# Kernel tuning notes

Hardware: AMD Instinct MI355X
Metric: run time of the kernel (lower is better)

The kernel has to match this reference:

```python
import jax, jax.numpy as jnp
import numpy as np

N_NODES = 50000
N_EDGES = 800000
IN_DIM = 128
ADD = 8
HIDDEN = 256
OUT_DIM = 128


def gcn_conv(x, src, dst, W, b, n_nodes):
    """PyG GCNConv: linear -> sym-normalized scatter-add with self-loops -> bias."""
    loop = jnp.arange(n_nodes, dtype=src.dtype)
    s = jnp.concatenate([src, loop])
    d = jnp.concatenate([dst, loop])
    deg = jax.ops.segment_sum(jnp.ones(s.shape[0], dtype=x.dtype), d, num_segments=n_nodes)
    dinv = jnp.where(deg > 0, jax.lax.rsqrt(deg), 0.0)
    norm = dinv[s] * dinv[d]                       # [E+N]
    h = x @ W                                      # [N, F_out]
    msg = h[s] * norm[:, None]                     # [E+N, F_out]
    out = jax.ops.segment_sum(msg, d, num_segments=n_nodes)
    return out + b


def prelu(x, a):
    return jnp.where(x >= 0, x, a * x)


def setup_inputs() -> dict:
    key = jax.random.key(0)
    ks = jax.random.split(key, 8)
    x = jax.random.normal(ks[0], (N_NODES, IN_DIM), dtype=jnp.float32)
    edge_index = jax.random.randint(ks[1], (2, N_EDGES), 0, N_NODES, dtype=jnp.int64)
    id_vec = jax.random.normal(ks[2], (ADD,), dtype=jnp.float32)
    # Glorot-ish init for linear weights, PReLU slope 0.25 (torch default)
    W1 = jax.random.normal(ks[3], (IN_DIM + ADD, HIDDEN), dtype=jnp.float32) * 0.05
    b1 = jnp.zeros((HIDDEN,), dtype=jnp.float32)
    a1 = jnp.full((HIDDEN,), 0.25, dtype=jnp.float32)
    W2 = jax.random.normal(ks[4], (HIDDEN, OUT_DIM), dtype=jnp.float32) * 0.05
    b2 = jnp.zeros((OUT_DIM,), dtype=jnp.float32)
    a2 = jnp.full((OUT_DIM,), 0.25, dtype=jnp.float32)
    return {"x": x, "edge_index": edge_index, "id": id_vec,
            "W1": W1, "b1": b1, "a1": a1, "W2": W2, "b2": b2, "a2": a2}


def reference(x, edge_index, id, W1, b1, a1, W2, b2, a2):
    n = x.shape[0]
    src, dst = edge_index[0], edge_index[1]
    # tile id vector onto every node and concat along features
    xi = jnp.concatenate([x, jnp.broadcast_to(id[None, :], (n, id.shape[0]))], axis=1)
    h = gcn_conv(xi, src, dst, W1, b1, n)
    h = prelu(h, a1)
    h = gcn_conv(h, src, dst, W2, b2, n)
    h = prelu(h, a2)
    return h
```

## Files before the change

kernel.cpp:

```cpp
#include <hip/hip_runtime.h>


constexpr int NN = 50000;
constexpr int NE = 800000;
constexpr int NBUCK = 196;
constexpr int TILE = 2048;
constexpr int NSCAT = (NE + TILE - 1) / TILE;

typedef __attribute__((ext_vector_type(8))) short short8;
typedef __attribute__((ext_vector_type(4))) float floatx4;

__device__ inline void bsplit(float v, unsigned short& hi, unsigned short& lo) {
  unsigned u = __float_as_uint(v);
  hi = (unsigned short)(u >> 16);
  float rem = v - __uint_as_float(u & 0xffff0000u);
  lo = (unsigned short)(__float_as_uint(rem) >> 16);
}

__device__ inline unsigned short bf16_rtne(float v) {
  unsigned u = __float_as_uint(v);
  return (unsigned short)((u + 0x7fffu + ((u >> 16) & 1u)) >> 16);
}

__device__ inline float bflo(unsigned u) { return __uint_as_float(u << 16); }
__device__ inline float bfhi(unsigned u) { return __uint_as_float(u & 0xffff0000u); }


__global__ __launch_bounds__(256) void tile_count_kernel(const int* __restrict__ ei,
                                                         int* __restrict__ tilecnt) {
  __shared__ int h[NBUCK];
  int t = threadIdx.x;
  for (int i = t; i < NBUCK; i += 256) h[i] = 0;
  __syncthreads();
  int base = blockIdx.x * TILE;
  int end = base + TILE; if (end > NE) end = NE;
  for (int e = base + t; e < end; e += 256) atomicAdd(&h[ei[NE + e] >> 8], 1);
  __syncthreads();
  for (int i = t; i < NBUCK; i += 256) tilecnt[blockIdx.x * NBUCK + i] = h[i];
}

__global__ __launch_bounds__(256) void tile_scan_a_kernel(const int* __restrict__ tilecnt,
                                                          int* __restrict__ tpre,
                                                          int* __restrict__ bcnt) {
  __shared__ int sm[256];
  int b = blockIdx.x, t = threadIdx.x;
  int i0 = 2 * t, i1 = 2 * t + 1;
  int v0 = (i0 < NSCAT) ? tilecnt[i0 * NBUCK + b] : 0;
  int v1 = (i1 < NSCAT) ? tilecnt[i1 * NBUCK + b] : 0;
  int s = v0 + v1;
  sm[t] = s;
  __syncthreads();
  for (int off = 1; off < 256; off <<= 1) {
    int u = (t >= off) ? sm[t - off] : 0;
    __syncthreads();
    sm[t] += u;
    __syncthreads();
  }
  int ex = sm[t] - s;
  if (i0 < NSCAT) tpre[i0 * NBUCK + b] = ex;
  if (i1 < NSCAT) tpre[i1 * NBUCK + b] = ex + v0;
  if (t == 255) bcnt[b] = sm[255];
}

__global__ void bucket_base_kernel(const int* __restrict__ bcnt, int* __restrict__ bbase) {
  __shared__ int sm[256];
  int t = threadIdx.x;
  int v = (t < NBUCK) ? bcnt[t] : 0;
  sm[t] = v;
  __syncthreads();
  for (int off = 1; off < 256; off <<= 1) {
    int u = (t >= off) ? sm[t - off] : 0;
    __syncthreads();
    sm[t] += u;
    __syncthreads();
  }
  if (t < NBUCK) bbase[t] = sm[t] - v;
}

__global__ __launch_bounds__(256) void bucket_scatter_kernel(
    const int* __restrict__ ei, const int* __restrict__ tilecnt,
    const int* __restrict__ tpre, const int* __restrict__ bbase,
    unsigned* __restrict__ ebuf) {
  __shared__ int lbase[NBUCK], gb[NBUCK], lcur[NBUCK], ssc[256];
  __shared__ unsigned stage[TILE];
  int t = threadIdx.x;
  int tile = blockIdx.x;
  int base = tile * TILE;
  int cntTile = NE - base; if (cntTile > TILE) cntTile = TILE;
  int h = (t < NBUCK) ? tilecnt[tile * NBUCK + t] : 0;
  ssc[t] = h;
  __syncthreads();
  for (int off = 1; off < 256; off <<= 1) {
    int u = (t >= off) ? ssc[t - off] : 0;
    __syncthreads();
    ssc[t] += u;
    __syncthreads();
  }
  if (t < NBUCK) {
    int ex = ssc[t] - h;
    lbase[t] = ex;
    lcur[t] = ex;
    gb[t] = bbase[t] + tpre[tile * NBUCK + t];
  }
  __syncthreads();
  for (int e = base + t; e < base + cntTile; e += 256) {
    int s = ei[e];
    int d = ei[NE + e];
    int b = d >> 8;
    int pos = atomicAdd(&lcur[b], 1);
    stage[pos] = ((unsigned)(d & 255) << 16) | (unsigned)s;
  }
  __syncthreads();
  for (int i = t; i < cntTile; i += 256) {
    int lo = 0, hi = NBUCK - 1;
    while (lo < hi) {
      int mid = (lo + hi + 1) >> 1;
      if (lbase[mid] <= i) lo = mid; else hi = mid - 1;
    }
    ebuf[gb[lo] + (i - lbase[lo])] = stage[i];
  }
}

__global__ __launch_bounds__(256) void bucket_csr_kernel(
    const unsigned* __restrict__ ebuf, const int* __restrict__ bbase,
    const int* __restrict__ bcnt, int* __restrict__ offs, int* __restrict__ col,
    float* __restrict__ dinv) {
  __shared__ int cnt[256], cur[256], sums[256];
  int b = blockIdx.x, t = threadIdx.x;
  int node0 = b << 8;
  cnt[t] = 0;
  __syncthreads();
  int g0 = bbase[b], g1 = g0 + bcnt[b];
  for (int i = g0 + t; i < g1; i += 256) atomicAdd(&cnt[ebuf[i] >> 16], 1);
  __syncthreads();
  int c = cnt[t];
  sums[t] = c;
  __syncthreads();
  for (int off = 1; off < 256; off <<= 1) {
    int u = (t >= off) ? sums[t - off] : 0;
    __syncthreads();
    sums[t] += u;
    __syncthreads();
  }
  int ex = sums[t] - c;
  cur[t] = ex;
  int node = node0 + t;
  if (node < NN) {
    offs[node] = g0 + ex;
    dinv[node] = rsqrtf((float)(c + 1));
  }
  __syncthreads();
  for (int i = g0 + t; i < g1; i += 256) {
    unsigned v = ebuf[i];
    int pos = atomicAdd(&cur[v >> 16], 1);
    col[g0 + pos] = (int)(v & 0xffffu);
  }
  if (b == 0 && t == 0) offs[NN] = NE;
}

__global__ __launch_bounds__(256) void post_csr_kernel(
    const float* __restrict__ x, const float* __restrict__ dinv,
    const int* __restrict__ offs, const int* __restrict__ col,
    unsigned short* __restrict__ xsb, float* __restrict__ Svec) {
  int id = blockIdx.x * 256 + threadIdx.x;
  if (id < NN * 32) {
    float dd = dinv[id >> 5];
    float4 v = ((const float4*)x)[id];
    ushort4 o;
    o.x = bf16_rtne(v.x * dd);
    o.y = bf16_rtne(v.y * dd);
    o.z = bf16_rtne(v.z * dd);
    o.w = bf16_rtne(v.w * dd);
    ((ushort4*)xsb)[id] = o;
  } else {
    int d = id - NN * 32;
    if (d < NN) {
      float s = 0.f;
      int end = offs[d + 1];
      for (int p = offs[d]; p < end; ++p) s += dinv[col[p]];
      float dd = dinv[d];
      Svec[d] = dd * (dd + s);
    }
  }
}

template <int K, int N>
__device__ inline void pack_one(const float* __restrict__ W, unsigned short* __restrict__ Bhi,
                                unsigned short* __restrict__ Blo, int id) {
  constexpr int KC = K / 32;
  int j = id & 7;
  int lane = (id >> 3) & 63;
  int rest = id >> 9;
  int c = rest % KC;
  int nt = rest / KC;
  int k = c * 32 + (lane >> 4) * 8 + j;
  int n = nt * 16 + (lane & 15);
  unsigned short hi, lo;
  bsplit(W[(size_t)k * N + n], hi, lo);
  Bhi[id] = hi;
  Blo[id] = lo;
}

__global__ void prep_weights_kernel(const float* __restrict__ W1, const float* __restrict__ W2,
                                    const float* __restrict__ idv,
                                    unsigned short* __restrict__ B1hi, unsigned short* __restrict__ B1lo,
                                    unsigned short* __restrict__ B2hi, unsigned short* __restrict__ B2lo,
                                    float* __restrict__ cvec) {
  int id = blockIdx.x * 256 + threadIdx.x;
  if (id < 32768) {
    pack_one<128, 256>(W1, B1hi, B1lo, id);
  } else if (id < 65536) {
    pack_one<256, 128>(W2, B2hi, B2lo, id - 32768);
  } else if (id < 65536 + 256) {
    int m = id - 65536;
    float c = 0.f;
#pragma unroll
    for (int j = 0; j < 8; ++j) c += idv[j] * W1[(128 + j) * 256 + m];
    cvec[m] = c;
  }
}

template <int MODE>
__global__ __launch_bounds__(256) void agg_kernel(
    const unsigned short* __restrict__ in, const float* __restrict__ dinv,
    const int* __restrict__ offs, const int* __restrict__ col,
    const float* __restrict__ bias, const float* __restrict__ alpha,
    unsigned short* __restrict__ outhi, unsigned short* __restrict__ outlo,
    float* __restrict__ outf) {
  const uint2* inb = (const uint2*)in;
  int t = threadIdx.x;
  int node = blockIdx.x * 4 + (t >> 6);
  int lane = t & 63;
  int r = lane & 31;
  int half = lane >> 5;
  int beg = offs[node], end = offs[node + 1];

  float4 a0 = make_float4(0.f, 0.f, 0.f, 0.f);
  float4 a1 = make_float4(0.f, 0.f, 0.f, 0.f);
  float4 a2 = make_float4(0.f, 0.f, 0.f, 0.f);
  float4 a3 = make_float4(0.f, 0.f, 0.f, 0.f);
  int p = beg + half;
  for (; p + 14 < end; p += 16) {
    int s0 = col[p];      int s1 = col[p + 2];
    int s2 = col[p + 4];  int s3 = col[p + 6];
    int s4 = col[p + 8];  int s5 = col[p + 10];
    int s6 = col[p + 12]; int s7 = col[p + 14];
    uint2 v0 = inb[(size_t)s0 * 32 + r];
    uint2 v1 = inb[(size_t)s1 * 32 + r];
    uint2 v2 = inb[(size_t)s2 * 32 + r];
    uint2 v3 = inb[(size_t)s3 * 32 + r];
    uint2 v4 = inb[(size_t)s4 * 32 + r];
    uint2 v5 = inb[(size_t)s5 * 32 + r];
    uint2 v6 = inb[(size_t)s6 * 32 + r];
    uint2 v7 = inb[(size_t)s7 * 32 + r];
    a0.x += bflo(v0.x); a0.y += bfhi(v0.x); a0.z += bflo(v0.y); a0.w += bfhi(v0.y);
    a1.x += bflo(v1.x); a1.y += bfhi(v1.x); a1.z += bflo(v1.y); a1.w += bfhi(v1.y);
    a2.x += bflo(v2.x); a2.y += bfhi(v2.x); a2.z += bflo(v2.y); a2.w += bfhi(v2.y);
    a3.x += bflo(v3.x); a3.y += bfhi(v3.x); a3.z += bflo(v3.y); a3.w += bfhi(v3.y);
    a0.x += bflo(v4.x); a0.y += bfhi(v4.x); a0.z += bflo(v4.y); a0.w += bfhi(v4.y);
    a1.x += bflo(v5.x); a1.y += bfhi(v5.x); a1.z += bflo(v5.y); a1.w += bfhi(v5.y);
    a2.x += bflo(v6.x); a2.y += bfhi(v6.x); a2.z += bflo(v6.y); a2.w += bfhi(v6.y);
    a3.x += bflo(v7.x); a3.y += bfhi(v7.x); a3.z += bflo(v7.y); a3.w += bfhi(v7.y);
  }
  for (; p + 2 < end; p += 4) {
    int s0 = col[p];
    int s1 = col[p + 2];
    uint2 v0 = inb[(size_t)s0 * 32 + r];
    uint2 v1 = inb[(size_t)s1 * 32 + r];
    a0.x += bflo(v0.x); a0.y += bfhi(v0.x); a0.z += bflo(v0.y); a0.w += bfhi(v0.y);
    a1.x += bflo(v1.x); a1.y += bfhi(v1.x); a1.z += bflo(v1.y); a1.w += bfhi(v1.y);
  }
  if (p < end) {
    uint2 v0 = inb[(size_t)col[p] * 32 + r];
    a0.x += bflo(v0.x); a0.y += bfhi(v0.x); a0.z += bflo(v0.y); a0.w += bfhi(v0.y);
  }
  float4 acc = make_float4((a0.x + a1.x) + (a2.x + a3.x), (a0.y + a1.y) + (a2.y + a3.y),
                           (a0.z + a1.z) + (a2.z + a3.z), (a0.w + a1.w) + (a2.w + a3.w));
  acc.x += __shfl_xor(acc.x, 32);
  acc.y += __shfl_xor(acc.y, 32);
  acc.z += __shfl_xor(acc.z, 32);
  acc.w += __shfl_xor(acc.w, 32);

  float dd = dinv[node];
  if (half == 0) {
    uint2 sv = inb[(size_t)node * 32 + r];
    acc.x = dd * (acc.x + bflo(sv.x));
    acc.y = dd * (acc.y + bfhi(sv.x));
    acc.z = dd * (acc.z + bflo(sv.y));
    acc.w = dd * (acc.w + bfhi(sv.y));
    if (MODE == 0) {
      ushort4 h4, l4;
      bsplit(acc.x, h4.x, l4.x);
      bsplit(acc.y, h4.y, l4.y);
      bsplit(acc.z, h4.z, l4.z);
      bsplit(acc.w, h4.w, l4.w);
      ((ushort4*)outhi)[(size_t)node * 32 + r] = h4;
      ((ushort4*)outlo)[(size_t)node * 32 + r] = l4;
    } else {
      float4 b = ((const float4*)bias)[r];
      float4 al = ((const float4*)alpha)[r];
      acc.x += b.x; acc.y += b.y; acc.z += b.z; acc.w += b.w;
      acc.x = (acc.x >= 0.f) ? acc.x : al.x * acc.x;
      acc.y = (acc.y >= 0.f) ? acc.y : al.y * acc.y;
      acc.z = (acc.z >= 0.f) ? acc.z : al.z * acc.z;
      acc.w = (acc.w >= 0.f) ? acc.w : al.w * acc.w;
      ((float4*)outf)[(size_t)node * 32 + r] = acc;
    }
  }
}

__global__ __launch_bounds__(256) void gemm_fused_kernel(
    const unsigned short* __restrict__ Ahi, const unsigned short* __restrict__ Alo,
    const unsigned short* __restrict__ B1hi, const unsigned short* __restrict__ B1lo,
    const unsigned short* __restrict__ B2hi, const unsigned short* __restrict__ B2lo,
    const float* __restrict__ Svec, const float* __restrict__ cvec,
    const float* __restrict__ bias, const float* __restrict__ alpha,
    const float* __restrict__ dinv, unsigned short* __restrict__ h2b) {
  constexpr int K1 = 128, KC1 = 4, NT1 = 16;
  constexpr int KC2 = 8, NT2 = 8;
  __shared__ __attribute__((aligned(16))) char smem[4 * 16384];

  int wave = threadIdx.x >> 6;
  int lane = threadIdx.x & 63;
  int row0 = blockIdx.x * 64 + wave * 16;
  if (row0 >= NN) return;
  int m = lane & 15, quad = lane >> 4;
  char* wb = smem + wave * 16384;

  short8 ah[KC1], al[KC1];
  const unsigned short* ap = Ahi + (size_t)(row0 + m) * K1 + quad * 8;
  const unsigned short* alp = Alo + (size_t)(row0 + m) * K1 + quad * 8;
#pragma unroll
  for (int c = 0; c < KC1; ++c) {
    ah[c] = *(const short8*)(ap + c * 32);
    al[c] = *(const short8*)(alp + c * 32);
  }
  float sv[4];
#pragma unroll
  for (int i = 0; i < 4; ++i) sv[i] = Svec[row0 + quad * 4 + i];

#pragma unroll 1
  for (int nt = 0; nt < NT1; ++nt) {
    floatx4 acc = {0.f, 0.f, 0.f, 0.f};
#pragma unroll
    for (int c = 0; c < KC1; ++c) {
      short8 bh = *(const short8*)(B1hi + ((size_t)(nt * KC1 + c) * 64 + lane) * 8);
      short8 bl = *(const short8*)(B1lo + ((size_t)(nt * KC1 + c) * 64 + lane) * 8);
      acc = __builtin_amdgcn_mfma_f32_16x16x32_bf16(ah[c], bh, acc, 0, 0, 0);
      acc = __builtin_amdgcn_mfma_f32_16x16x32_bf16(ah[c], bl, acc, 0, 0, 0);
      acc = __builtin_amdgcn_mfma_f32_16x16x32_bf16(al[c], bh, acc, 0, 0, 0);
    }
    int c0 = nt * 16 + m;
    float cv = cvec[c0], bb = bias[c0], aa = alpha[c0];
#pragma unroll
    for (int i = 0; i < 4; ++i) {
      float v = acc[i] + sv[i] * cv + bb;
      v = (v >= 0.f) ? v : aa * v;
      unsigned short hi, lo;
      bsplit(v, hi, lo);
      int row16 = quad * 4 + i;
      int off = row16 * 512 + ((c0 * 2) ^ ((row16 & 7) << 4));
      *(unsigned short*)(wb + off) = hi;
      *(unsigned short*)(wb + 8192 + off) = lo;
    }
  }

  short8 ah2[KC2], al2[KC2];
#pragma unroll
  for (int c = 0; c < KC2; ++c) {
    int off = m * 512 + ((c * 64 + quad * 16) ^ ((m & 7) << 4));
    ah2[c] = *(const short8*)(wb + off);
    al2[c] = *(const short8*)(wb + 8192 + off);
  }
  float dv[4];
#pragma unroll
  for (int i = 0; i < 4; ++i) dv[i] = dinv[row0 + quad * 4 + i];

#pragma unroll 1
  for (int nt = 0; nt < NT2; ++nt) {
    floatx4 acc = {0.f, 0.f, 0.f, 0.f};
#pragma unroll
    for (int c = 0; c < KC2; ++c) {
      short8 bh = *(const short8*)(B2hi + ((size_t)(nt * KC2 + c) * 64 + lane) * 8);
      short8 bl = *(const short8*)(B2lo + ((size_t)(nt * KC2 + c) * 64 + lane) * 8);
      acc = __builtin_amdgcn_mfma_f32_16x16x32_bf16(ah2[c], bh, acc, 0, 0, 0);
      acc = __builtin_amdgcn_mfma_f32_16x16x32_bf16(ah2[c], bl, acc, 0, 0, 0);
      acc = __builtin_amdgcn_mfma_f32_16x16x32_bf16(al2[c], bh, acc, 0, 0, 0);
    }
    int c0 = nt * 16 + m;
#pragma unroll
    for (int i = 0; i < 4; ++i) {
      int r = row0 + quad * 4 + i;
      h2b[(size_t)r * 128 + c0] = bf16_rtne(acc[i] * dv[i]);
    }
  }
}

extern "C" void kernel_launch(void* const* d_in, const int* in_sizes, int n_in,
                              void* d_out, int out_size, void* d_ws, size_t ws_size,
                              hipStream_t stream) {
  const float* x = (const float*)d_in[0];
  const int* ei = (const int*)d_in[1];
  const float* idv = (const float*)d_in[2];
  const float* W1 = (const float*)d_in[3];
  const float* b1 = (const float*)d_in[4];
  const float* a1 = (const float*)d_in[5];
  const float* W2 = (const float*)d_in[6];
  const float* b2 = (const float*)d_in[7];
  const float* a2 = (const float*)d_in[8];
  float* out = (float*)d_out;

  char* w = (char*)d_ws;
  size_t off = 0;
  auto alloc = [&](size_t bytes) -> void* {
    void* p = w + off;
    off += bytes;
    off = (off + 255) & ~(size_t)255;
    return p;
  };
  int* tilecnt = (int*)alloc((size_t)NSCAT * NBUCK * 4);
  int* tpre = (int*)alloc((size_t)NSCAT * NBUCK * 4);
  int* bbase = (int*)alloc((size_t)NBUCK * 4);
  int* bcnt = (int*)alloc((size_t)NBUCK * 4);
  unsigned* ebuf = (unsigned*)alloc((size_t)NE * 4);
  float* dinv = (float*)alloc((size_t)NN * 4);
  float* Svec = (float*)alloc((size_t)NN * 4);
  int* offs = (int*)alloc((size_t)(NN + 1) * 4);
  int* col = (int*)alloc((size_t)NE * 4);
  float* cvec = (float*)alloc(256 * 4);
  unsigned short* xsb = (unsigned short*)alloc((size_t)NN * 128 * 2);
  unsigned short* aggxhi = (unsigned short*)alloc((size_t)NN * 128 * 2);
  unsigned short* aggxlo = (unsigned short*)alloc((size_t)NN * 128 * 2);
  unsigned short* h2b = (unsigned short*)alloc((size_t)NN * 128 * 2);
  unsigned short* B1hi = (unsigned short*)alloc(128 * 256 * 2);
  unsigned short* B1lo = (unsigned short*)alloc(128 * 256 * 2);
  unsigned short* B2hi = (unsigned short*)alloc(256 * 128 * 2);
  unsigned short* B2lo = (unsigned short*)alloc(256 * 128 * 2);

  tile_count_kernel<<<NSCAT, 256, 0, stream>>>(ei, tilecnt);
  tile_scan_a_kernel<<<NBUCK, 256, 0, stream>>>(tilecnt, tpre, bcnt);
  bucket_base_kernel<<<1, 256, 0, stream>>>(bcnt, bbase);
  bucket_scatter_kernel<<<NSCAT, 256, 0, stream>>>(ei, tilecnt, tpre, bbase, ebuf);
  bucket_csr_kernel<<<NBUCK, 256, 0, stream>>>(ebuf, bbase, bcnt, offs, col, dinv);

  prep_weights_kernel<<<(65536 + 256 + 255) / 256, 256, 0, stream>>>(
      W1, W2, idv, B1hi, B1lo, B2hi, B2lo, cvec);
  post_csr_kernel<<<(NN * 32 + NN + 255) / 256, 256, 0, stream>>>(
      x, dinv, offs, col, xsb, Svec);

  agg_kernel<0><<<NN / 4, 256, 0, stream>>>(xsb, dinv, offs, col, nullptr, nullptr,
                                            aggxhi, aggxlo, nullptr);

  gemm_fused_kernel<<<(NN + 63) / 64, 256, 0, stream>>>(
      aggxhi, aggxlo, B1hi, B1lo, B2hi, B2lo, Svec, cvec, b1, a1, dinv, h2b);

  agg_kernel<1><<<NN / 4, 256, 0, stream>>>(h2b, dinv, offs, col, b2, a2,
                                            nullptr, nullptr, out);
}
```

Baseline: 256.4 us.

## Chain fused GEMMs in registers via transposed MFMA, removing LDS staging

Swaps the MFMA operand roles so the first GEMM produces a transposed output tile whose per-lane layout matches the B-operand layout of the second GEMM. W1 is repacked with a permuted column order so that each pair of 16-column tiles feeds one 32-wide K chunk of the second GEMM directly from registers. This drops the per-wave 16KB LDS staging buffer and lets output stores be vectorized ushort4 writes. In exchange it keeps eight accumulator tiles live across the loop, which raises register pressure, and it adds a launch_bounds occupancy hint.

```diff
diff --git a/kernel.cpp b/kernel.cpp
--- a/kernel.cpp
+++ b/kernel.cpp
@@ -201,6 +201,22 @@
   Blo[id] = lo;
 }
 
+__device__ inline void pack_w1(const float* __restrict__ W, unsigned short* __restrict__ Bhi,
+                               unsigned short* __restrict__ Blo, int id) {
+  int j = id & 7;
+  int lane = (id >> 3) & 63;
+  int rest = id >> 9;
+  int c = rest & 3;
+  int nt = rest >> 2;
+  int k = c * 32 + (lane >> 4) * 8 + j;
+  int r = lane & 15;
+  int n = 32 * (nt >> 1) + 8 * (r >> 2) + 4 * (nt & 1) + (r & 3);
+  unsigned short hi, lo;
+  bsplit(W[(size_t)k * 256 + n], hi, lo);
+  Bhi[id] = hi;
+  Blo[id] = lo;
+}
+
 __global__ void prep_weights_kernel(const float* __restrict__ W1, const float* __restrict__ W2,
                                     const float* __restrict__ idv,
                                     unsigned short* __restrict__ B1hi, unsigned short* __restrict__ B1lo,
@@ -208,7 +224,7 @@
                                     float* __restrict__ cvec) {
   int id = blockIdx.x * 256 + threadIdx.x;
   if (id < 32768) {
-    pack_one<128, 256>(W1, B1hi, B1lo, id);
+    pack_w1(W1, B1hi, B1lo, id);
   } else if (id < 65536) {
     pack_one<256, 128>(W2, B2hi, B2lo, id - 32768);
   } else if (id < 65536 + 256) {
@@ -309,90 +325,89 @@
   }
 }
 
-__global__ __launch_bounds__(256) void gemm_fused_kernel(
+__global__ __launch_bounds__(256, 4) void gemm_fused_kernel(
     const unsigned short* __restrict__ Ahi, const unsigned short* __restrict__ Alo,
     const unsigned short* __restrict__ B1hi, const unsigned short* __restrict__ B1lo,
     const unsigned short* __restrict__ B2hi, const unsigned short* __restrict__ B2lo,
     const float* __restrict__ Svec, const float* __restrict__ cvec,
     const float* __restrict__ bias, const float* __restrict__ alpha,
     const float* __restrict__ dinv, unsigned short* __restrict__ h2b) {
-  constexpr int K1 = 128, KC1 = 4, NT1 = 16;
-  constexpr int KC2 = 8, NT2 = 8;
-  __shared__ __attribute__((aligned(16))) char smem[4 * 16384];
-
+  constexpr int K1 = 128, KC1 = 4;
   int wave = threadIdx.x >> 6;
   int lane = threadIdx.x & 63;
   int row0 = blockIdx.x * 64 + wave * 16;
   if (row0 >= NN) return;
   int m = lane & 15, quad = lane >> 4;
-  char* wb = smem + wave * 16384;
-
-  short8 ah[KC1], al[KC1];
-  const unsigned short* ap = Ahi + (size_t)(row0 + m) * K1 + quad * 8;
-  const unsigned short* alp = Alo + (size_t)(row0 + m) * K1 + quad * 8;
+  int node = row0 + m;
+
+  short8 gh[KC1], gl[KC1];
+  const unsigned short* gp = Ahi + (size_t)node * K1 + quad * 8;
+  const unsigned short* glp = Alo + (size_t)node * K1 + quad * 8;
 #pragma unroll
   for (int c = 0; c < KC1; ++c) {
-    ah[c] = *(const short8*)(ap + c * 32);
-    al[c] = *(const short8*)(alp + c * 32);
-  }
-  float sv[4];
-#pragma unroll
-  for (int i = 0; i < 4; ++i) sv[i] = Svec[row0 + quad * 4 + i];
+    gh[c] = *(const short8*)(gp + c * 32);
+    gl[c] = *(const short8*)(glp + c * 32);
+  }
+  float sv = Svec[node];
+  float dv = dinv[node];
+
+  floatx4 acc2[8];
+#pragma unroll
+  for (int n = 0; n < 8; ++n) acc2[n] = {0.f, 0.f, 0.f, 0.f};
 
 #pragma unroll 1
-  for (int nt = 0; nt < NT1; ++nt) {
-    floatx4 acc = {0.f, 0.f, 0.f, 0.f};
-#pragma unroll
-    for (int c = 0; c < KC1; ++c) {
-      short8 bh = *(const short8*)(B1hi + ((size_t)(nt * KC1 + c) * 64 + lane) * 8);
-      short8 bl = *(const short8*)(B1lo + ((size_t)(nt * KC1 + c) * 64 + lane) * 8);
-      acc = __builtin_amdgcn_mfma_f32_16x16x32_bf16(ah[c], bh, acc, 0, 0, 0);
-      acc = __builtin_amdgcn_mfma_f32_16x16x32_bf16(ah[c], bl, acc, 0, 0, 0);
-      acc = __builtin_amdgcn_mfma_f32_16x16x32_bf16(al[c], bh, acc, 0, 0, 0);
-    }
-    int c0 = nt * 16 + m;
-    float cv = cvec[c0], bb = bias[c0], aa = alpha[c0];
+  for (int t = 0; t < 8; ++t) {
+    float p0[4], p1[4];
+#pragma unroll
+    for (int P = 0; P < 2; ++P) {
+      int nt = 2 * t + P;
+      floatx4 acc = {0.f, 0.f, 0.f, 0.f};
+#pragma unroll
+      for (int c = 0; c < KC1; ++c) {
+        short8 wh = *(const short8*)(B1hi + ((size_t)(nt * KC1 + c) * 64 + lane) * 8);
+        short8 wl = *(const short8*)(B1lo + ((size_t)(nt * KC1 + c) * 64 + lane) * 8);
+        acc = __builtin_amdgcn_mfma_f32_16x16x32_bf16(wh, gh[c], acc, 0, 0, 0);
+        acc = __builtin_amdgcn_mfma_f32_16x16x32_bf16(wl, gh[c], acc, 0, 0, 0);
+        acc = __builtin_amdgcn_mfma_f32_16x16x32_bf16(wh, gl[c], acc, 0, 0, 0);
+      }
+      int cb = t * 32 + quad * 8 + P * 4;
+      floatx4 cvv = *(const floatx4*)(cvec + cb);
+      floatx4 bbv = *(const floatx4*)(bias + cb);
+      floatx4 aav = *(const floatx4*)(alpha + cb);
+#pragma unroll
+      for (int i = 0; i < 4; ++i) {
+        float v = acc[i] + sv * cvv[i] + bbv[i];
+        v = (v >= 0.f) ? v : aav[i] * v;
+        if (P == 0) p0[i] = v; else p1[i] = v;
+      }
+    }
+    short8 bh2, bl2;
 #pragma unroll
     for (int i = 0; i < 4; ++i) {
-      float v = acc[i] + sv[i] * cv + bb;
-      v = (v >= 0.f) ? v : aa * v;
       unsigned short hi, lo;
-      bsplit(v, hi, lo);
-      int row16 = quad * 4 + i;
-      int off = row16 * 512 + ((c0 * 2) ^ ((row16 & 7) << 4));
-      *(unsigned short*)(wb + off) = hi;
-      *(unsigned short*)(wb + 8192 + off) = lo;
-    }
-  }
-
-  short8 ah2[KC2], al2[KC2];
-#pragma unroll
-  for (int c = 0; c < KC2; ++c) {
-    int off = m * 512 + ((c * 64 + quad * 16) ^ ((m & 7) << 4));
-    ah2[c] = *(const short8*)(wb + off);
-    al2[c] = *(const short8*)(wb + 8192 + off);
-  }
-  float dv[4];
-#pragma unroll
-  for (int i = 0; i < 4; ++i) dv[i] = dinv[row0 + quad * 4 + i];
-
-#pragma unroll 1
-  for (int nt = 0; nt < NT2; ++nt) {
-    floatx4 acc = {0.f, 0.f, 0.f, 0.f};
-#pragma unroll
-    for (int c = 0; c < KC2; ++c) {
-      short8 bh = *(const short8*)(B2hi + ((size_t)(nt * KC2 + c) * 64 + lane) * 8);
-      short8 bl = *(const short8*)(B2lo + ((size_t)(nt * KC2 + c) * 64 + lane) * 8);
-      acc = __builtin_amdgcn_mfma_f32_16x16x32_bf16(ah2[c], bh, acc, 0, 0, 0);
-      acc = __builtin_amdgcn_mfma_f32_16x16x32_bf16(ah2[c], bl, acc, 0, 0, 0);
-      acc = __builtin_amdgcn_mfma_f32_16x16x32_bf16(al2[c], bh, acc, 0, 0, 0);
-    }
-    int c0 = nt * 16 + m;
-#pragma unroll
-    for (int i = 0; i < 4; ++i) {
-      int r = row0 + quad * 4 + i;
-      h2b[(size_t)r * 128 + c0] = bf16_rtne(acc[i] * dv[i]);
-    }
+      bsplit(p0[i], hi, lo);
+      bh2[i] = (short)hi; bl2[i] = (short)lo;
+      bsplit(p1[i], hi, lo);
+      bh2[4 + i] = (short)hi; bl2[4 + i] = (short)lo;
+    }
+#pragma unroll
+    for (int n = 0; n < 8; ++n) {
+      short8 a2h = *(const short8*)(B2hi + ((size_t)(n * 8 + t) * 64 + lane) * 8);
+      short8 a2l = *(const short8*)(B2lo + ((size_t)(n * 8 + t) * 64 + lane) * 8);
+      acc2[n] = __builtin_amdgcn_mfma_f32_16x16x32_bf16(a2h, bh2, acc2[n], 0, 0, 0);
+      acc2[n] = __builtin_amdgcn_mfma_f32_16x16x32_bf16(a2l, bh2, acc2[n], 0, 0, 0);
+      acc2[n] = __builtin_amdgcn_mfma_f32_16x16x32_bf16(a2h, bl2, acc2[n], 0, 0, 0);
+    }
+  }
+
+#pragma unroll
+  for (int n = 0; n < 8; ++n) {
+    ushort4 o;
+    o.x = bf16_rtne(acc2[n][0] * dv);
+    o.y = bf16_rtne(acc2[n][1] * dv);
+    o.z = bf16_rtne(acc2[n][2] * dv);
+    o.w = bf16_rtne(acc2[n][3] * dv);
+    *(ushort4*)(h2b + (size_t)node * 128 + n * 16 + quad * 4) = o;
   }
 }
 
```

New measurement: 274.4 us. 7.0% more time.

## Fuse first-layer neighbor aggregation into the fused GEMM kernel via LDS staging

Applied to the files above, without the earlier changes.

The separate first aggregation kernel, which wrote hi/lo bf16 split buffers to global memory, is removed. Each wave of the GEMM kernel now gathers its own 16 rows from the CSR, splits the results into hi/lo and stores them in a swizzled LDS tile, then loads the MFMA A operands from LDS. This drops one launch and the global write plus read-back of two 50000x128 bf16 buffers. In exchange, each wave walks 16 nodes one after another, so the gather has less parallelism per wave and its latency is harder to hide, and it now runs inside a kernel with high register pressure.

```diff
diff --git a/kernel.cpp b/kernel.cpp
--- a/kernel.cpp
+++ b/kernel.cpp
@@ -220,12 +220,10 @@
   }
 }
 
-template <int MODE>
 __global__ __launch_bounds__(256) void agg_kernel(
     const unsigned short* __restrict__ in, const float* __restrict__ dinv,
     const int* __restrict__ offs, const int* __restrict__ col,
     const float* __restrict__ bias, const float* __restrict__ alpha,
-    unsigned short* __restrict__ outhi, unsigned short* __restrict__ outlo,
     float* __restrict__ outf) {
   const uint2* inb = (const uint2*)in;
   int t = threadIdx.x;
@@ -283,57 +281,117 @@
 
   float dd = dinv[node];
   if (half == 0) {
-    uint2 sv = inb[(size_t)node * 32 + r];
-    acc.x = dd * (acc.x + bflo(sv.x));
-    acc.y = dd * (acc.y + bfhi(sv.x));
-    acc.z = dd * (acc.z + bflo(sv.y));
-    acc.w = dd * (acc.w + bfhi(sv.y));
-    if (MODE == 0) {
+    uint2 slf = inb[(size_t)node * 32 + r];
+    acc.x = dd * (acc.x + bflo(slf.x));
+    acc.y = dd * (acc.y + bfhi(slf.x));
+    acc.z = dd * (acc.z + bflo(slf.y));
+    acc.w = dd * (acc.w + bfhi(slf.y));
+    float4 b = ((const float4*)bias)[r];
+    float4 al = ((const float4*)alpha)[r];
+    acc.x += b.x; acc.y += b.y; acc.z += b.z; acc.w += b.w;
+    acc.x = (acc.x >= 0.f) ? acc.x : al.x * acc.x;
+    acc.y = (acc.y >= 0.f) ? acc.y : al.y * acc.y;
+    acc.z = (acc.z >= 0.f) ? acc.z : al.z * acc.z;
+    acc.w = (acc.w >= 0.f) ? acc.w : al.w * acc.w;
+    ((float4*)outf)[(size_t)node * 32 + r] = acc;
+  }
+}
+
+__global__ __launch_bounds__(256) void gemm_fused_kernel(
+    const unsigned short* __restrict__ xsb, const int* __restrict__ offs,
+    const int* __restrict__ col,
+    const unsigned short* __restrict__ B1hi, const unsigned short* __restrict__ B1lo,
+    const unsigned short* __restrict__ B2hi, const unsigned short* __restrict__ B2lo,
+    const float* __restrict__ Svec, const float* __restrict__ cvec,
+    const float* __restrict__ bias, const float* __restrict__ alpha,
+    const float* __restrict__ dinv, unsigned short* __restrict__ h2b) {
+  constexpr int KC1 = 4, NT1 = 16;
+  constexpr int KC2 = 8, NT2 = 8;
+  __shared__ __attribute__((aligned(16))) char smem[4 * 16384];
+
+  int wave = threadIdx.x >> 6;
+  int lane = threadIdx.x & 63;
+  int row0 = blockIdx.x * 64 + wave * 16;
+  if (row0 >= NN) return;
+  int m = lane & 15, quad = lane >> 4;
+  int r = lane & 31, half = lane >> 5;
+  char* wb = smem + wave * 16384;
+  const uint2* inb = (const uint2*)xsb;
+
+#pragma unroll 1
+  for (int i = 0; i < 16; ++i) {
+    int node = row0 + i;
+    int beg = offs[node], end = offs[node + 1];
+    float4 a0 = make_float4(0.f, 0.f, 0.f, 0.f);
+    float4 a1 = make_float4(0.f, 0.f, 0.f, 0.f);
+    float4 a2 = make_float4(0.f, 0.f, 0.f, 0.f);
+    float4 a3 = make_float4(0.f, 0.f, 0.f, 0.f);
+    int p = beg + half;
+    for (; p + 14 < end; p += 16) {
+      int s0 = col[p];      int s1 = col[p + 2];
+      int s2 = col[p + 4];  int s3 = col[p + 6];
+      int s4 = col[p + 8];  int s5 = col[p + 10];
+      int s6 = col[p + 12]; int s7 = col[p + 14];
+      uint2 v0 = inb[(size_t)s0 * 32 + r];
+      uint2 v1 = inb[(size_t)s1 * 32 + r];
+      uint2 v2 = inb[(size_t)s2 * 32 + r];
+      uint2 v3 = inb[(size_t)s3 * 32 + r];
+      uint2 v4 = inb[(size_t)s4 * 32 + r];
+      uint2 v5 = inb[(size_t)s5 * 32 + r];
+      uint2 v6 = inb[(size_t)s6 * 32 + r];
+      uint2 v7 = inb[(size_t)s7 * 32 + r];
+      a0.x += bflo(v0.x); a0.y += bfhi(v0.x); a0.z += bflo(v0.y); a0.w += bfhi(v0.y);
+      a1.x += bflo(v1.x); a1.y += bfhi(v1.x); a1.z += bflo(v1.y); a1.w += bfhi(v1.y);
+      a2.x += bflo(v2.x); a2.y += bfhi(v2.x); a2.z += bflo(v2.y); a2.w += bfhi(v2.y);
+      a3.x += bflo(v3.x); a3.y += bfhi(v3.x); a3.z += bflo(v3.y); a3.w += bfhi(v3.y);
+      a0.x += bflo(v4.x); a0.y += bfhi(v4.x); a0.z += bflo(v4.y); a0.w += bfhi(v4.y);
+      a1.x += bflo(v5.x); a1.y += bfhi(v5.x); a1.z += bflo(v5.y); a1.w += bfhi(v5.y);
+      a2.x += bflo(v6.x); a2.y += bfhi(v6.x); a2.z += bflo(v6.y); a2.w += bfhi(v6.y);
+      a3.x += bflo(v7.x); a3.y += bfhi(v7.x); a3.z += bflo(v7.y); a3.w += bfhi(v7.y);
+    }
+    for (; p + 2 < end; p += 4) {
+      int s0 = col[p];
+      int s1 = col[p + 2];
+      uint2 v0 = inb[(size_t)s0 * 32 + r];
+      uint2 v1 = inb[(size_t)s1 * 32 + r];
+      a0.x += bflo(v0.x); a0.y += bfhi(v0.x); a0.z += bflo(v0.y); a0.w += bfhi(v0.y);
+      a1.x += bflo(v1.x); a1.y += bfhi(v1.x); a1.z += bflo(v1.y); a1.w += bfhi(v1.y);
+    }
+    if (p < end) {
+      uint2 v0 = inb[(size_t)col[p] * 32 + r];
+      a0.x += bflo(v0.x); a0.y += bfhi(v0.x); a0.z += bflo(v0.y); a0.w += bfhi(v0.y);
+    }
+    float4 acc = make_float4((a0.x + a1.x) + (a2.x + a3.x), (a0.y + a1.y) + (a2.y + a3.y),
+                             (a0.z + a1.z) + (a2.z + a3.z), (a0.w + a1.w) + (a2.w + a3.w));
+    acc.x += __shfl_xor(acc.x, 32);
+    acc.y += __shfl_xor(acc.y, 32);
+    acc.z += __shfl_xor(acc.z, 32);
+    acc.w += __shfl_xor(acc.w, 32);
+
+    float dd = dinv[node];
+    if (half == 0) {
+      uint2 slf = inb[(size_t)node * 32 + r];
+      acc.x = dd * (acc.x + bflo(slf.x));
+      acc.y = dd * (acc.y + bfhi(slf.x));
+      acc.z = dd * (acc.z + bflo(slf.y));
+      acc.w = dd * (acc.w + bfhi(slf.y));
       ushort4 h4, l4;
       bsplit(acc.x, h4.x, l4.x);
       bsplit(acc.y, h4.y, l4.y);
       bsplit(acc.z, h4.z, l4.z);
       bsplit(acc.w, h4.w, l4.w);
-      ((ushort4*)outhi)[(size_t)node * 32 + r] = h4;
-      ((ushort4*)outlo)[(size_t)node * 32 + r] = l4;
-    } else {
-      float4 b = ((const float4*)bias)[r];
-      float4 al = ((const float4*)alpha)[r];
-      acc.x += b.x; acc.y += b.y; acc.z += b.z; acc.w += b.w;
-      acc.x = (acc.x >= 0.f) ? acc.x : al.x * acc.x;
-      acc.y = (acc.y >= 0.f) ? acc.y : al.y * acc.y;
-      acc.z = (acc.z >= 0.f) ? acc.z : al.z * acc.z;
-      acc.w = (acc.w >= 0.f) ? acc.w : al.w * acc.w;
-      ((float4*)outf)[(size_t)node * 32 + r] = acc;
-    }
-  }
-}
-
-__global__ __launch_bounds__(256) void gemm_fused_kernel(
-    const unsigned short* __restrict__ Ahi, const unsigned short* __restrict__ Alo,
-    const unsigned short* __restrict__ B1hi, const unsigned short* __restrict__ B1lo,
-    const unsigned short* __restrict__ B2hi, const unsigned short* __restrict__ B2lo,
-    const float* __restrict__ Svec, const float* __restrict__ cvec,
-    const float* __restrict__ bias, const float* __restrict__ alpha,
-    const float* __restrict__ dinv, unsigned short* __restrict__ h2b) {
-  constexpr int K1 = 128, KC1 = 4, NT1 = 16;
-  constexpr int KC2 = 8, NT2 = 8;
-  __shared__ __attribute__((aligned(16))) char smem[4 * 16384];
-
-  int wave = threadIdx.x >> 6;
-  int lane = threadIdx.x & 63;
-  int row0 = blockIdx.x * 64 + wave * 16;
-  if (row0 >= NN) return;
-  int m = lane & 15, quad = lane >> 4;
-  char* wb = smem + wave * 16384;
+      int loff = i * 256 + ((r * 8) ^ ((i & 7) << 4));
+      *(ushort4*)(wb + loff) = h4;
+      *(ushort4*)(wb + 4096 + loff) = l4;
+    }
+  }
 
   short8 ah[KC1], al[KC1];
-  const unsigned short* ap = Ahi + (size_t)(row0 + m) * K1 + quad * 8;
-  const unsigned short* alp = Alo + (size_t)(row0 + m) * K1 + quad * 8;
 #pragma unroll
   for (int c = 0; c < KC1; ++c) {
-    ah[c] = *(const short8*)(ap + c * 32);
-    al[c] = *(const short8*)(alp + c * 32);
+    int loff = m * 256 + ((c * 64 + quad * 16) ^ ((m & 7) << 4));
+    ah[c] = *(const short8*)(wb + loff);
+    al[c] = *(const short8*)(wb + 4096 + loff);
   }
   float sv[4];
 #pragma unroll
@@ -390,8 +448,8 @@
     int c0 = nt * 16 + m;
 #pragma unroll
     for (int i = 0; i < 4; ++i) {
-      int r = row0 + quad * 4 + i;
-      h2b[(size_t)r * 128 + c0] = bf16_rtne(acc[i] * dv[i]);
+      int rr = row0 + quad * 4 + i;
+      h2b[(size_t)rr * 128 + c0] = bf16_rtne(acc[i] * dv[i]);
     }
   }
 }
@@ -429,8 +487,6 @@
   int* col = (int*)alloc((size_t)NE * 4);
   float* cvec = (float*)alloc(256 * 4);
   unsigned short* xsb = (unsigned short*)alloc((size_t)NN * 128 * 2);
-  unsigned short* aggxhi = (unsigned short*)alloc((size_t)NN * 128 * 2);
-  unsigned short* aggxlo = (unsigned short*)alloc((size_t)NN * 128 * 2);
   unsigned short* h2b = (unsigned short*)alloc((size_t)NN * 128 * 2);
   unsigned short* B1hi = (unsigned short*)alloc(128 * 256 * 2);
   unsigned short* B1lo = (unsigned short*)alloc(128 * 256 * 2);
@@ -448,12 +504,8 @@
   post_csr_kernel<<<(NN * 32 + NN + 255) / 256, 256, 0, stream>>>(
       x, dinv, offs, col, xsb, Svec);
 
-  agg_kernel<0><<<NN / 4, 256, 0, stream>>>(xsb, dinv, offs, col, nullptr, nullptr,
-                                            aggxhi, aggxlo, nullptr);
-
   gemm_fused_kernel<<<(NN + 63) / 64, 256, 0, stream>>>(
-      aggxhi, aggxlo, B1hi, B1lo, B2hi, B2lo, Svec, cvec, b1, a1, dinv, h2b);
-
-  agg_kernel<1><<<NN / 4, 256, 0, stream>>>(h2b, dinv, offs, col, b2, a2,
-                                            nullptr, nullptr, out);
-}
+      xsb, offs, col, B1hi, B1lo, B2hi, B2lo, Svec, cvec, b1, a1, dinv, h2b);
+
+  agg_kernel<<<NN / 4, 256, 0, stream>>>(h2b, dinv, offs, col, b2, a2, out);
+}
```

Result: slower. 308.5 us (+20.3%).

## Merge CSR build and preprocessing kernels into one cooperative kernel with grid syncs

Applied to the files above, without the earlier changes.

Replaces seven separate launches (tile count, scans, bucket scatter, CSR build, weight packing, x scaling/Svec) with a single cooperative kernel of NSCAT blocks that separates phases with grid.sync. The goal is to remove per-launch overhead and inter-kernel gaps in the graph-preprocessing stage. In exchange, the post-CSR elementwise work now runs on only ~391 blocks via grid-stride loops instead of a wide grid, and each grid barrier has its own cost.

```diff
diff --git a/kernel.cpp b/kernel.cpp
--- a/kernel.cpp
+++ b/kernel.cpp
@@ -1,4 +1,7 @@
 #include <hip/hip_runtime.h>
+#include <hip/hip_cooperative_groups.h>
+
+namespace cg = cooperative_groups;
 
 
 constexpr int NN = 50000;
@@ -6,6 +9,7 @@
 constexpr int NBUCK = 196;
 constexpr int TILE = 2048;
 constexpr int NSCAT = (NE + TILE - 1) / TILE;
+constexpr int GTH = NSCAT * 256;
 
 typedef __attribute__((ext_vector_type(8))) short short8;
 typedef __attribute__((ext_vector_type(4))) float floatx4;
@@ -24,165 +28,6 @@
 
 __device__ inline float bflo(unsigned u) { return __uint_as_float(u << 16); }
 __device__ inline float bfhi(unsigned u) { return __uint_as_float(u & 0xffff0000u); }
-
-
-__global__ __launch_bounds__(256) void tile_count_kernel(const int* __restrict__ ei,
-                                                         int* __restrict__ tilecnt) {
-  __shared__ int h[NBUCK];
-  int t = threadIdx.x;
-  for (int i = t; i < NBUCK; i += 256) h[i] = 0;
-  __syncthreads();
-  int base = blockIdx.x * TILE;
-  int end = base + TILE; if (end > NE) end = NE;
-  for (int e = base + t; e < end; e += 256) atomicAdd(&h[ei[NE + e] >> 8], 1);
-  __syncthreads();
-  for (int i = t; i < NBUCK; i += 256) tilecnt[blockIdx.x * NBUCK + i] = h[i];
-}
-
-__global__ __launch_bounds__(256) void tile_scan_a_kernel(const int* __restrict__ tilecnt,
-                                                          int* __restrict__ tpre,
-                                                          int* __restrict__ bcnt) {
-  __shared__ int sm[256];
-  int b = blockIdx.x, t = threadIdx.x;
-  int i0 = 2 * t, i1 = 2 * t + 1;
-  int v0 = (i0 < NSCAT) ? tilecnt[i0 * NBUCK + b] : 0;
-  int v1 = (i1 < NSCAT) ? tilecnt[i1 * NBUCK + b] : 0;
-  int s = v0 + v1;
-  sm[t] = s;
-  __syncthreads();
-  for (int off = 1; off < 256; off <<= 1) {
-    int u = (t >= off) ? sm[t - off] : 0;
-    __syncthreads();
-    sm[t] += u;
-    __syncthreads();
-  }
-  int ex = sm[t] - s;
-  if (i0 < NSCAT) tpre[i0 * NBUCK + b] = ex;
-  if (i1 < NSCAT) tpre[i1 * NBUCK + b] = ex + v0;
-  if (t == 255) bcnt[b] = sm[255];
-}
-
-__global__ void bucket_base_kernel(const int* __restrict__ bcnt, int* __restrict__ bbase) {
-  __shared__ int sm[256];
-  int t = threadIdx.x;
-  int v = (t < NBUCK) ? bcnt[t] : 0;
-  sm[t] = v;
-  __syncthreads();
-  for (int off = 1; off < 256; off <<= 1) {
-    int u = (t >= off) ? sm[t - off] : 0;
-    __syncthreads();
-    sm[t] += u;
-    __syncthreads();
-  }
-  if (t < NBUCK) bbase[t] = sm[t] - v;
-}
-
-__global__ __launch_bounds__(256) void bucket_scatter_kernel(
-    const int* __restrict__ ei, const int* __restrict__ tilecnt,
-    const int* __restrict__ tpre, const int* __restrict__ bbase,
-    unsigned* __restrict__ ebuf) {
-  __shared__ int lbase[NBUCK], gb[NBUCK], lcur[NBUCK], ssc[256];
-  __shared__ unsigned stage[TILE];
-  int t = threadIdx.x;
-  int tile = blockIdx.x;
-  int base = tile * TILE;
-  int cntTile = NE - base; if (cntTile > TILE) cntTile = TILE;
-  int h = (t < NBUCK) ? tilecnt[tile * NBUCK + t] : 0;
-  ssc[t] = h;
-  __syncthreads();
-  for (int off = 1; off < 256; off <<= 1) {
-    int u = (t >= off) ? ssc[t - off] : 0;
-    __syncthreads();
-    ssc[t] += u;
-    __syncthreads();
-  }
-  if (t < NBUCK) {
-    int ex = ssc[t] - h;
-    lbase[t] = ex;
-    lcur[t] = ex;
-    gb[t] = bbase[t] + tpre[tile * NBUCK + t];
-  }
-  __syncthreads();
-  for (int e = base + t; e < base + cntTile; e += 256) {
-    int s = ei[e];
-    int d = ei[NE + e];
-    int b = d >> 8;
-    int pos = atomicAdd(&lcur[b], 1);
-    stage[pos] = ((unsigned)(d & 255) << 16) | (unsigned)s;
-  }
-  __syncthreads();
-  for (int i = t; i < cntTile; i += 256) {
-    int lo = 0, hi = NBUCK - 1;
-    while (lo < hi) {
-      int mid = (lo + hi + 1) >> 1;
-      if (lbase[mid] <= i) lo = mid; else hi = mid - 1;
-    }
-    ebuf[gb[lo] + (i - lbase[lo])] = stage[i];
-  }
-}
-
-__global__ __launch_bounds__(256) void bucket_csr_kernel(
-    const unsigned* __restrict__ ebuf, const int* __restrict__ bbase,
-    const int* __restrict__ bcnt, int* __restrict__ offs, int* __restrict__ col,
-    float* __restrict__ dinv) {
-  __shared__ int cnt[256], cur[256], sums[256];
-  int b = blockIdx.x, t = threadIdx.x;
-  int node0 = b << 8;
-  cnt[t] = 0;
-  __syncthreads();
-  int g0 = bbase[b], g1 = g0 + bcnt[b];
-  for (int i = g0 + t; i < g1; i += 256) atomicAdd(&cnt[ebuf[i] >> 16], 1);
-  __syncthreads();
-  int c = cnt[t];
-  sums[t] = c;
-  __syncthreads();
-  for (int off = 1; off < 256; off <<= 1) {
-    int u = (t >= off) ? sums[t - off] : 0;
-    __syncthreads();
-    sums[t] += u;
-    __syncthreads();
-  }
-  int ex = sums[t] - c;
-  cur[t] = ex;
-  int node = node0 + t;
-  if (node < NN) {
-    offs[node] = g0 + ex;
-    dinv[node] = rsqrtf((float)(c + 1));
-  }
-  __syncthreads();
-  for (int i = g0 + t; i < g1; i += 256) {
-    unsigned v = ebuf[i];
-    int pos = atomicAdd(&cur[v >> 16], 1);
-    col[g0 + pos] = (int)(v & 0xffffu);
-  }
-  if (b == 0 && t == 0) offs[NN] = NE;
-}
-
-__global__ __launch_bounds__(256) void post_csr_kernel(
-    const float* __restrict__ x, const float* __restrict__ dinv,
-    const int* __restrict__ offs, const int* __restrict__ col,
-    unsigned short* __restrict__ xsb, float* __restrict__ Svec) {
-  int id = blockIdx.x * 256 + threadIdx.x;
-  if (id < NN * 32) {
-    float dd = dinv[id >> 5];
-    float4 v = ((const float4*)x)[id];
-    ushort4 o;
-    o.x = bf16_rtne(v.x * dd);
-    o.y = bf16_rtne(v.y * dd);
-    o.z = bf16_rtne(v.z * dd);
-    o.w = bf16_rtne(v.w * dd);
-    ((ushort4*)xsb)[id] = o;
-  } else {
-    int d = id - NN * 32;
-    if (d < NN) {
-      float s = 0.f;
-      int end = offs[d + 1];
-      for (int p = offs[d]; p < end; ++p) s += dinv[col[p]];
-      float dd = dinv[d];
-      Svec[d] = dd * (dd + s);
-    }
-  }
-}
 
 template <int K, int N>
 __device__ inline void pack_one(const float* __restrict__ W, unsigned short* __restrict__ Bhi,
@@ -201,22 +46,184 @@
   Blo[id] = lo;
 }
 
-__global__ void prep_weights_kernel(const float* __restrict__ W1, const float* __restrict__ W2,
-                                    const float* __restrict__ idv,
-                                    unsigned short* __restrict__ B1hi, unsigned short* __restrict__ B1lo,
-                                    unsigned short* __restrict__ B2hi, unsigned short* __restrict__ B2lo,
-                                    float* __restrict__ cvec) {
-  int id = blockIdx.x * 256 + threadIdx.x;
-  if (id < 32768) {
-    pack_one<128, 256>(W1, B1hi, B1lo, id);
-  } else if (id < 65536) {
-    pack_one<256, 128>(W2, B2hi, B2lo, id - 32768);
-  } else if (id < 65536 + 256) {
-    int m = id - 65536;
-    float c = 0.f;
-#pragma unroll
-    for (int j = 0; j < 8; ++j) c += idv[j] * W1[(128 + j) * 256 + m];
-    cvec[m] = c;
+__global__ __launch_bounds__(256) void build_kernel(
+    const int* __restrict__ ei, const float* __restrict__ x,
+    const float* __restrict__ W1, const float* __restrict__ W2,
+    const float* __restrict__ idv,
+    int* __restrict__ tilecnt, int* __restrict__ tpre, int* __restrict__ bbase,
+    int* __restrict__ bcnt, unsigned* __restrict__ ebuf,
+    int* __restrict__ offs, int* __restrict__ col, float* __restrict__ dinv,
+    unsigned short* __restrict__ xsb, float* __restrict__ Svec,
+    unsigned short* __restrict__ B1hi, unsigned short* __restrict__ B1lo,
+    unsigned short* __restrict__ B2hi, unsigned short* __restrict__ B2lo,
+    float* __restrict__ cvec) {
+  cg::grid_group grid = cg::this_grid();
+  __shared__ __attribute__((aligned(16))) char shraw[12288];
+  int t = threadIdx.x;
+  int blk = blockIdx.x;
+
+  for (int id = blk * 256 + t; id < 65536 + 256; id += GTH) {
+    if (id < 32768) {
+      pack_one<128, 256>(W1, B1hi, B1lo, id);
+    } else if (id < 65536) {
+      pack_one<256, 128>(W2, B2hi, B2lo, id - 32768);
+    } else {
+      int m = id - 65536;
+      float c = 0.f;
+#pragma unroll
+      for (int j = 0; j < 8; ++j) c += idv[j] * W1[(128 + j) * 256 + m];
+      cvec[m] = c;
+    }
+  }
+
+  {
+    int* h = (int*)shraw;
+    for (int i = t; i < NBUCK; i += 256) h[i] = 0;
+    __syncthreads();
+    int base = blk * TILE;
+    int end = base + TILE; if (end > NE) end = NE;
+    for (int e = base + t; e < end; e += 256) atomicAdd(&h[ei[NE + e] >> 8], 1);
+    __syncthreads();
+    for (int i = t; i < NBUCK; i += 256) tilecnt[blk * NBUCK + i] = h[i];
+  }
+  grid.sync();
+
+  if (blk < NBUCK) {
+    int* sm = (int*)shraw;
+    int b = blk;
+    int i0 = 2 * t, i1 = 2 * t + 1;
+    int v0 = (i0 < NSCAT) ? tilecnt[i0 * NBUCK + b] : 0;
+    int v1 = (i1 < NSCAT) ? tilecnt[i1 * NBUCK + b] : 0;
+    int s = v0 + v1;
+    sm[t] = s;
+    __syncthreads();
+    for (int off = 1; off < 256; off <<= 1) {
+      int u = (t >= off) ? sm[t - off] : 0;
+      __syncthreads();
+      sm[t] += u;
+      __syncthreads();
+    }
+    int ex = sm[t] - s;
+    if (i0 < NSCAT) tpre[i0 * NBUCK + b] = ex;
+    if (i1 < NSCAT) tpre[i1 * NBUCK + b] = ex + v0;
+    if (t == 255) bcnt[b] = sm[255];
+  }
+  grid.sync();
+
+  if (blk == 0) {
+    int* sm = (int*)shraw;
+    int v = (t < NBUCK) ? bcnt[t] : 0;
+    sm[t] = v;
+    __syncthreads();
+    for (int off = 1; off < 256; off <<= 1) {
+      int u = (t >= off) ? sm[t - off] : 0;
+      __syncthreads();
+      sm[t] += u;
+      __syncthreads();
+    }
+    if (t < NBUCK) bbase[t] = sm[t] - v;
+  }
+  grid.sync();
+
+  {
+    int* lbase = (int*)shraw;
+    int* gb = lbase + NBUCK;
+    int* lcur = gb + NBUCK;
+    int* ssc = lcur + NBUCK;
+    unsigned* stage = (unsigned*)(ssc + 256);
+    int tile = blk;
+    int base = tile * TILE;
+    int cntTile = NE - base; if (cntTile > TILE) cntTile = TILE;
+    int h = (t < NBUCK) ? tilecnt[tile * NBUCK + t] : 0;
+    ssc[t] = h;
+    __syncthreads();
+    for (int off = 1; off < 256; off <<= 1) {
+      int u = (t >= off) ? ssc[t - off] : 0;
+      __syncthreads();
+      ssc[t] += u;
+      __syncthreads();
+    }
+    if (t < NBUCK) {
+      int ex = ssc[t] - h;
+      lbase[t] = ex;
+      lcur[t] = ex;
+      gb[t] = bbase[t] + tpre[tile * NBUCK + t];
+    }
+    __syncthreads();
+    for (int e = base + t; e < base + cntTile; e += 256) {
+      int s = ei[e];
+      int d = ei[NE + e];
+      int b = d >> 8;
+      int pos = atomicAdd(&lcur[b], 1);
+      stage[pos] = ((unsigned)(d & 255) << 16) | (unsigned)s;
+    }
+    __syncthreads();
+    for (int i = t; i < cntTile; i += 256) {
+      int lo = 0, hi = NBUCK - 1;
+      while (lo < hi) {
+        int mid = (lo + hi + 1) >> 1;
+        if (lbase[mid] <= i) lo = mid; else hi = mid - 1;
+      }
+      ebuf[gb[lo] + (i - lbase[lo])] = stage[i];
+    }
+  }
+  grid.sync();
+
+  if (blk < NBUCK) {
+    int* cnt = (int*)shraw;
+    int* cur = cnt + 256;
+    int* sums = cur + 256;
+    int b = blk;
+    int node0 = b << 8;
+    cnt[t] = 0;
+    __syncthreads();
+    int g0 = bbase[b], g1 = g0 + bcnt[b];
+    for (int i = g0 + t; i < g1; i += 256) atomicAdd(&cnt[ebuf[i] >> 16], 1);
+    __syncthreads();
+    int c = cnt[t];
+    sums[t] = c;
+    __syncthreads();
+    for (int off = 1; off < 256; off <<= 1) {
+      int u = (t >= off) ? sums[t - off] : 0;
+      __syncthreads();
+      sums[t] += u;
+      __syncthreads();
+    }
+    int ex = sums[t] - c;
+    cur[t] = ex;
+    int node = node0 + t;
+    if (node < NN) {
+      offs[node] = g0 + ex;
+      dinv[node] = rsqrtf((float)(c + 1));
+    }
+    __syncthreads();
+    for (int i = g0 + t; i < g1; i += 256) {
+      unsigned v = ebuf[i];
+      int pos = atomicAdd(&cur[v >> 16], 1);
+      col[g0 + pos] = (int)(v & 0xffffu);
+    }
+    if (b == 0 && t == 0) offs[NN] = NE;
+  }
+  grid.sync();
+
+  for (int id = blk * 256 + t; id < NN * 32 + NN; id += GTH) {
+    if (id < NN * 32) {
+      float dd = dinv[id >> 5];
+      float4 v = ((const float4*)x)[id];
+      ushort4 o;
+      o.x = bf16_rtne(v.x * dd);
+      o.y = bf16_rtne(v.y * dd);
+      o.z = bf16_rtne(v.z * dd);
+      o.w = bf16_rtne(v.w * dd);
+      ((ushort4*)xsb)[id] = o;
+    } else {
+      int d = id - NN * 32;
+      float s = 0.f;
+      int end = offs[d + 1];
+      for (int p = offs[d]; p < end; ++p) s += dinv[col[p]];
+      float dd = dinv[d];
+      Svec[d] = dd * (dd + s);
+    }
   }
 }
 
@@ -437,16 +444,13 @@
   unsigned short* B2hi = (unsigned short*)alloc(256 * 128 * 2);
   unsigned short* B2lo = (unsigned short*)alloc(256 * 128 * 2);
 
-  tile_count_kernel<<<NSCAT, 256, 0, stream>>>(ei, tilecnt);
-  tile_scan_a_kernel<<<NBUCK, 256, 0, stream>>>(tilecnt, tpre, bcnt);
-  bucket_base_kernel<<<1, 256, 0, stream>>>(bcnt, bbase);
-  bucket_scatter_kernel<<<NSCAT, 256, 0, stream>>>(ei, tilecnt, tpre, bbase, ebuf);
-  bucket_csr_kernel<<<NBUCK, 256, 0, stream>>>(ebuf, bbase, bcnt, offs, col, dinv);
-
-  prep_weights_kernel<<<(65536 + 256 + 255) / 256, 256, 0, stream>>>(
-      W1, W2, idv, B1hi, B1lo, B2hi, B2lo, cvec);
-  post_csr_kernel<<<(NN * 32 + NN + 255) / 256, 256, 0, stream>>>(
-      x, dinv, offs, col, xsb, Svec);
+  void* args[] = {(void*)&ei, (void*)&x, (void*)&W1, (void*)&W2, (void*)&idv,
+                  (void*)&tilecnt, (void*)&tpre, (void*)&bbase, (void*)&bcnt,
+                  (void*)&ebuf, (void*)&offs, (void*)&col, (void*)&dinv,
+                  (void*)&xsb, (void*)&Svec, (void*)&B1hi, (void*)&B1lo,
+                  (void*)&B2hi, (void*)&B2lo, (void*)&cvec};
+  hipLaunchCooperativeKernel((void*)build_kernel, dim3(NSCAT), dim3(256),
+                             args, 0, stream);
 
   agg_kernel<0><<<NN / 4, 256, 0, stream>>>(xsb, dinv, offs, col, nullptr, nullptr,
                                             aggxhi, aggxlo, nullptr);
```

After: 482.9 us. +88.4%, slower.
